# Kernel tuning notes

Hardware: AMD Instinct MI355X
Metric: run time of the kernel (lower is better)

The kernel has to match this reference:

```python
import jax, jax.numpy as jnp
import numpy as np

MAX_RADIUS = 0.9
TEMP = 0.1

def _to_poincare(x, W, b):
    # Linear + Tanh, then rescale into Poincare ball of radius 0.9
    h = jnp.tanh(x @ W.T + b)
    norm = jnp.clip(jnp.linalg.norm(h, axis=-1, keepdims=True), 1e-8, None)
    scale = jnp.where(norm > MAX_RADIUS, MAX_RADIUS / norm, jnp.ones_like(norm))
    return h * scale

def setup_inputs() -> dict:
    key = jax.random.key(0)
    kq, kw, kb, km, ko = jax.random.split(key, 5)
    B, N, D = 2048, 100000, 128
    return {
        "query": jax.random.normal(kq, (B, D), dtype=jnp.float32),
        "W": jax.random.normal(kw, (D, D), dtype=jnp.float32) * (1.0 / np.sqrt(D)),
        "b": jax.random.normal(kb, (D,), dtype=jnp.float32) * 0.01,
        "mem_emb": jax.random.normal(km, (N, D), dtype=jnp.float32),
        "mem_out": jax.random.normal(ko, (N, D), dtype=jnp.float32),
        "k": 16,
    }

def reference(query, W, b, mem_emb, mem_out, k):
    q = _to_poincare(query, W, b)          # [B, D]
    m = _to_poincare(mem_emb, W, b)        # [N, D]
    # Euclidean cdist via the GEMM form: ||q||^2 + ||m||^2 - 2 q.m
    q2 = jnp.sum(q * q, axis=-1, keepdims=True)           # [B, 1]
    m2 = jnp.sum(m * m, axis=-1)                          # [N]
    d2 = q2 + m2[None, :] - 2.0 * (q @ m.T)               # [B, N]
    dists = jnp.sqrt(jnp.maximum(d2, 1e-12))
    # k smallest distances
    neg_top, top_idx = jax.lax.top_k(-dists, k)           # [B, k]
    top_dists = -neg_top
    weights = jax.nn.softmax(-top_dists / TEMP, axis=-1)  # [B, k]
    outcomes = mem_out[top_idx]                           # [B, k, D]
    return weights, outcomes
```

## Files before the change

### kernel.cpp

```cpp
#include <hip/hip_runtime.h>
#include <hip/hip_bf16.h>
#include <math.h>

#define DIM 128
#define QB 64
#define MB 64
#define NSPLIT 32
#define KSEL 16
#define KOWN 4
#define RESCORE 32
#define IDXMASK 0x1FFFu
#define KEYMASK 0xFFFFE000u

using bf16x8 = __attribute__((ext_vector_type(8))) short;
using f32x4  = __attribute__((ext_vector_type(4))) float;

__device__ inline unsigned short f2bf(float f) {
  __hip_bfloat16 h = __float2bfloat16(f);
  return __builtin_bit_cast(unsigned short, h);
}
__device__ inline unsigned uminu(unsigned a, unsigned b) {
  return __builtin_elementwise_min(a, b);
}
__device__ inline unsigned umaxu(unsigned a, unsigned b) {
  return __builtin_elementwise_max(a, b);
}
__device__ inline unsigned long long umin64(unsigned long long a,
                                            unsigned long long b) {
  return __builtin_elementwise_min(a, b);
}

__device__ inline f32x4 mfma16(bf16x8 a, bf16x8 b, f32x4 c) {
  return __builtin_amdgcn_mfma_f32_16x16x32_bf16(a, b, c, 0, 0, 0);
}

__device__ inline void gload_lds16(const void* g, void* l) {
  __builtin_amdgcn_global_load_lds(
      (const __attribute__((address_space(1))) void*)g,
      (__attribute__((address_space(3))) void*)l, 16, 0, 0);
}

__global__ __launch_bounds__(512) void poincare2_k(
    const float* __restrict__ Xm, int Rm,
    const float* __restrict__ Xq, int Rq,
    const float* __restrict__ W, const float* __restrict__ bias,
    float* __restrict__ Pm, float* __restrict__ Pm2,
    float* __restrict__ Pm2s, int npadm,
    unsigned short* __restrict__ Pmbf,
    float* __restrict__ Pq, float* __restrict__ Pq2, int nbm)
{
  __shared__ float Wl[DIM * DIM];
  __shared__ float nrm[128 * 17];
  __shared__ float norm2l[128];

  const int t  = threadIdx.x;
  const int cg = t & 15;
  const int rg = t >> 4;

  const bool ismem = (int)blockIdx.x < nbm;
  const float* X = ismem ? Xm : Xq;
  const int    R = ismem ? Rm : Rq;
  float*       P  = ismem ? Pm  : Pq;
  float*       P2 = ismem ? Pm2 : Pq2;
  unsigned short* Pbf = ismem ? Pmbf : nullptr;
  const int rbase = (ismem ? blockIdx.x : (blockIdx.x - nbm)) * 128;

  for (int i = t; i < DIM * 32; i += 512) {
    const int j = i >> 5, c = i & 31;
    const float4 v = *(const float4*)&W[j * DIM + c * 4];
    *(float4*)&Wl[j * DIM + ((c ^ ((j >> 3) & 7)) << 2)] = v;
  }
  float bj[8];
  #pragma unroll
  for (int u = 0; u < 8; ++u) bj[u] = bias[cg * 8 + u];

  const float* xr[4];
  #pragma unroll
  for (int v = 0; v < 4; ++v) {
    int row = rbase + rg + 32 * v;
    if (row > R - 1) row = R - 1;
    xr[v] = X + (size_t)row * DIM;
  }
  __syncthreads();

  float acc[4][8];
  #pragma unroll
  for (int v = 0; v < 4; ++v)
    #pragma unroll
    for (int u = 0; u < 8; ++u) acc[v][u] = bj[u];

  #pragma unroll 2
  for (int k4 = 0; k4 < 32; ++k4) {
    float4 xv[4], wv[8];
    #pragma unroll
    for (int v = 0; v < 4; ++v) xv[v] = *(const float4*)&xr[v][k4 * 4];
    #pragma unroll
    for (int u = 0; u < 8; ++u) {
      const int j = cg * 8 + u;
      wv[u] = *(const float4*)&Wl[j * DIM + ((k4 ^ ((j >> 3) & 7)) << 2)];
    }
    #pragma unroll
    for (int v = 0; v < 4; ++v)
      #pragma unroll
      for (int u = 0; u < 8; ++u) {
        acc[v][u] = fmaf(xv[v].x, wv[u].x, acc[v][u]);
        acc[v][u] = fmaf(xv[v].y, wv[u].y, acc[v][u]);
        acc[v][u] = fmaf(xv[v].z, wv[u].z, acc[v][u]);
        acc[v][u] = fmaf(xv[v].w, wv[u].w, acc[v][u]);
      }
  }

  #pragma unroll
  for (int v = 0; v < 4; ++v) {
    float pn = 0.f;
    #pragma unroll
    for (int u = 0; u < 8; ++u) {
      const float th = tanhf(acc[v][u]);
      acc[v][u] = th;
      pn = fmaf(th, th, pn);
    }
    nrm[(rg + 32 * v) * 17 + cg] = pn;
  }
  __syncthreads();
  if (t < 128) {
    float s = 0.f;
    #pragma unroll
    for (int c2 = 0; c2 < 16; ++c2) s += nrm[t * 17 + c2];
    norm2l[t] = s;
    const int row = rbase + t;
    if (row < R) {
      const float nm = sqrtf(s);
      const float sc = (nm > 0.9f) ? (0.9f / nm) : 1.0f;
      const float p2v = s * sc * sc;
      P2[row] = p2v;
      if (ismem) Pm2s[row] = fmaf(0.5f, p2v, 1.0f);
    } else if (ismem && row < npadm) {
      Pm2s[row] = __int_as_float(0x7f800000);
    }
  }
  __syncthreads();

  #pragma unroll
  for (int v = 0; v < 4; ++v) {
    const int r = rg + 32 * v;
    const int row = rbase + r;
    if (row < R) {
      const float n2 = norm2l[r];
      const float nm = sqrtf(n2);
      const float sc = (nm > 0.9f) ? (0.9f / nm) : 1.0f;
      float o[8];
      #pragma unroll
      for (int u = 0; u < 8; ++u) o[u] = acc[v][u] * sc;
      *(float4*)&P[(size_t)row * DIM + cg * 8]     = make_float4(o[0], o[1], o[2], o[3]);
      *(float4*)&P[(size_t)row * DIM + cg * 8 + 4] = make_float4(o[4], o[5], o[6], o[7]);
      if (Pbf) {
        uint4 pb;
        pb.x = (unsigned)f2bf(o[0]) | ((unsigned)f2bf(o[1]) << 16);
        pb.y = (unsigned)f2bf(o[2]) | ((unsigned)f2bf(o[3]) << 16);
        pb.z = (unsigned)f2bf(o[4]) | ((unsigned)f2bf(o[5]) << 16);
        pb.w = (unsigned)f2bf(o[6]) | ((unsigned)f2bf(o[7]) << 16);
        *(uint4*)&Pmbf[(size_t)row * DIM + ((cg ^ (row & 15)) << 3)] = pb;
      }
    }
  }
}

template<bool USEBF>
__global__ __launch_bounds__(512, 8) void score_topk_k(
    const float* __restrict__ Pq,
    const float* __restrict__ Pm, const float* __restrict__ Pm2s,
    const unsigned short* __restrict__ Pmbf,
    int N, int splitlen, unsigned* __restrict__ splitTop)
{
  __shared__ __align__(16) unsigned short Ml0[MB * DIM];
  __shared__ __align__(16) unsigned short Ml1[MB * DIM];

  const int t = threadIdx.x;
  const int lane = t & 63;
  const int w = t >> 6, wr = w >> 1, wc = w & 1;
  const int split = blockIdx.x;
  const int qbase = blockIdx.y * QB;
  const int mlo = split * splitlen;
  const int mhi = min(mlo + splitlen, N);

  bf16x8 qf[4];
  {
    const int qrow = qbase + wr * 16 + (lane & 15);
    #pragma unroll
    for (int ks = 0; ks < 4; ++ks) {
      const float* src = &Pq[(size_t)qrow * DIM + ks * 32 + (lane >> 4) * 8];
      float4 lo = *(const float4*)src;
      float4 hi = *(const float4*)(src + 4);
      bf16x8 v;
      v[0] = (short)f2bf(-lo.x); v[1] = (short)f2bf(-lo.y);
      v[2] = (short)f2bf(-lo.z); v[3] = (short)f2bf(-lo.w);
      v[4] = (short)f2bf(-hi.x); v[5] = (short)f2bf(-hi.y);
      v[6] = (short)f2bf(-hi.z); v[7] = (short)f2bf(-hi.w);
      qf[ks] = v;
    }
  }

  const size_t soff0 = (size_t)(w * 8 + (lane >> 4)) * DIM + ((lane & 15) << 3);
  const size_t soff1 = soff0 + 4 * DIM;
  unsigned short* const d00 = &Ml0[(w * 8) * DIM];
  unsigned short* const d01 = &Ml0[(w * 8 + 4) * DIM];
  unsigned short* const d10 = &Ml1[(w * 8) * DIM];
  unsigned short* const d11 = &Ml1[(w * 8 + 4) * DIM];

  auto stage = [&](int mbase, unsigned short* dA, unsigned short* dB,
                   unsigned short* lds) {
    if constexpr (USEBF) {
      const unsigned short* b = Pmbf + (size_t)mbase * DIM;
      gload_lds16(b + soff0, dA);
      gload_lds16(b + soff1, dB);
    } else {
      const int fr = t >> 3, fe = t & 7;
      const float* src = Pm + (size_t)(mbase + fr) * DIM + fe * 16;
      float4 a0 = *(const float4*)(src + 0);
      float4 a1 = *(const float4*)(src + 4);
      float4 a2 = *(const float4*)(src + 8);
      float4 a3 = *(const float4*)(src + 12);
      uint4 o0, o1;
      o0.x = (unsigned)f2bf(a0.x) | ((unsigned)f2bf(a0.y) << 16);
      o0.y = (unsigned)f2bf(a0.z) | ((unsigned)f2bf(a0.w) << 16);
      o0.z = (unsigned)f2bf(a1.x) | ((unsigned)f2bf(a1.y) << 16);
      o0.w = (unsigned)f2bf(a1.z) | ((unsigned)f2bf(a1.w) << 16);
      o1.x = (unsigned)f2bf(a2.x) | ((unsigned)f2bf(a2.y) << 16);
      o1.y = (unsigned)f2bf(a2.z) | ((unsigned)f2bf(a2.w) << 16);
      o1.z = (unsigned)f2bf(a3.x) | ((unsigned)f2bf(a3.y) << 16);
      o1.w = (unsigned)f2bf(a3.z) | ((unsigned)f2bf(a3.w) << 16);
      char* base = (char*)lds + fr * 256;
      *(uint4*)(base + (((2 * fe)     ^ (fr & 15)) << 4)) = o0;
      *(uint4*)(base + (((2 * fe + 1) ^ (fr & 15)) << 4)) = o1;
    }
  };

  const int ntiles = (mhi - mlo + MB - 1) / MB;
  const int mcol = wc * 32 + (lane & 15);

  stage(mlo, d00, d01, Ml0);
  float ca = Pm2s[mlo + mcol];
  float cb = Pm2s[mlo + mcol + 16];
  float caN, cbN;
  __syncthreads();

  unsigned keys[4][KOWN];
  #pragma unroll
  for (int r = 0; r < 4; ++r)
    #pragma unroll
    for (int i = 0; i < KOWN; ++i) keys[r][i] = 0xFFFFFFFFu;

  auto body = [&](int tile, const unsigned short* ldsCur,
                  unsigned short* dA, unsigned short* dB, unsigned short* ldsNxt,
                  float ca_, float cb_, float& caN_, float& cbN_) {
    const int mbase = mlo + tile * MB;
    const bool more = (tile + 1 < ntiles);
    if (more) {
      stage(mbase + MB, dA, dB, ldsNxt);
      caN_ = Pm2s[mbase + MB + mcol];
      cbN_ = Pm2s[mbase + MB + mcol + 16];
    }

    f32x4 acc0 = (f32x4){ca_, ca_, ca_, ca_};
    f32x4 acc1 = (f32x4){cb_, cb_, cb_, cb_};

    const int rowA = mcol;
    const int rowB = mcol + 16;
    __builtin_amdgcn_s_setprio(1);
    #pragma unroll
    for (int ks = 0; ks < 4; ++ks) {
      const int kb = ks * 64 + (lane >> 4) * 16;
      bf16x8 bfrA = *(const bf16x8*)((const char*)ldsCur + rowA * 256 +
                                     (kb ^ ((rowA & 15) << 4)));
      bf16x8 bfrB = *(const bf16x8*)((const char*)ldsCur + rowB * 256 +
                                     (kb ^ ((rowB & 15) << 4)));
      acc0 = mfma16(qf[ks], bfrA, acc0);
      acc1 = mfma16(qf[ks], bfrB, acc1);
    }
    __builtin_amdgcn_s_setprio(0);

    const unsigned idx0 = (unsigned)(tile * MB + mcol);
    #pragma unroll
    for (int r = 0; r < 4; ++r) {
      {
        unsigned c = (__float_as_uint(acc0[r]) & KEYMASK) | idx0;
        #pragma unroll
        for (int i = 0; i < KOWN; ++i) {
          const unsigned lo = uminu(c, keys[r][i]);
          c = umaxu(c, keys[r][i]);
          keys[r][i] = lo;
        }
      }
      {
        unsigned c = (__float_as_uint(acc1[r]) & KEYMASK) | (idx0 + 16);
        #pragma unroll
        for (int i = 0; i < KOWN; ++i) {
          const unsigned lo = uminu(c, keys[r][i]);
          c = umaxu(c, keys[r][i]);
          keys[r][i] = lo;
        }
      }
    }
    __syncthreads();
  };

  int tile = 0;
  while (true) {
    body(tile, Ml0, d10, d11, Ml1, ca, cb, caN, cbN); if (++tile == ntiles) break;
    body(tile, Ml1, d00, d01, Ml0, caN, cbN, ca, cb); if (++tile == ntiles) break;
  }

  #pragma unroll
  for (int r = 0; r < 4; ++r) {
    unsigned k0 = keys[r][0], k1 = keys[r][1];
    unsigned k2 = keys[r][2], k3 = keys[r][3];
    unsigned out = 0xFFFFFFFFu;
    for (int round = 0; round < 8; ++round) {
      unsigned g = k0;
      g = uminu(g, __shfl_xor(g, 1, 16));
      g = uminu(g, __shfl_xor(g, 2, 16));
      g = uminu(g, __shfl_xor(g, 4, 16));
      g = uminu(g, __shfl_xor(g, 8, 16));
      const bool mine = (k0 == g);
      k0 = mine ? k1 : k0;
      k1 = mine ? k2 : k1;
      k2 = mine ? k3 : k2;
      k3 = mine ? 0xFFFFFFFFu : k3;
      if ((lane & 15) == round) out = g;
    }
    const int q = qbase + wr * 16 + (lane >> 4) * 4 + r;
    if ((lane & 15) < 8)
      splitTop[(((size_t)q * NSPLIT + split) * 2 + wc) * 8 + (lane & 15)] = out;
  }
}

__global__ __launch_bounds__(256) void finalize_k(
    const unsigned* __restrict__ splitTop,
    const float* __restrict__ Pq, const float* __restrict__ Pq2,
    const float* __restrict__ Pm, const float* __restrict__ Pm2,
    const float* __restrict__ memOut, int N, int splitlen,
    float* __restrict__ outW, float* __restrict__ outO)
{
  const int wv   = threadIdx.x >> 6;
  const int lane = threadIdx.x & 63;
  const int q = blockIdx.x * 4 + wv;

  __shared__ unsigned      sKey[4][RESCORE];
  __shared__ unsigned char sSrc[4][RESCORE];
  __shared__ unsigned long long sKeyx[4][RESCORE];
  __shared__ unsigned long long sSel[4][KSEL];
  __shared__ float sEl[4][KSEL];

  {
    const unsigned* gp = splitTop + (size_t)q * (NSPLIT * 2 * 8) + lane * 8;
    unsigned a[8];
    uint4 lo = *(const uint4*)gp;
    uint4 hi = *(const uint4*)(gp + 4);
    a[0] = lo.x; a[1] = lo.y; a[2] = lo.z; a[3] = lo.w;
    a[4] = hi.x; a[5] = hi.y; a[6] = hi.z; a[7] = hi.w;
    for (int r = 0; r < RESCORE; ++r) {
      unsigned g = a[0];
      g = uminu(g, __shfl_xor(g, 1));
      g = uminu(g, __shfl_xor(g, 2));
      g = uminu(g, __shfl_xor(g, 4));
      g = uminu(g, __shfl_xor(g, 8));
      g = uminu(g, __shfl_xor(g, 16));
      g = uminu(g, __shfl_xor(g, 32));
      unsigned long long mask = __ballot(a[0] == g);
      const int fl = __ffsll((unsigned long long)mask) - 1;
      if (lane == fl) {
        #pragma unroll
        for (int i = 0; i < 7; ++i) a[i] = a[i + 1];
        a[7] = 0xFFFFFFFFu;
      }
      if (lane == 0) { sKey[wv][r] = g; sSrc[wv][r] = (unsigned char)fl; }
    }
  }

  #pragma unroll
  for (int p = 0; p < 4; ++p) {
    const int g8 = p * 8 + (lane >> 3), e = lane & 7;
    const int src = sSrc[wv][g8];
    const int gidx = (src >> 1) * splitlen + (int)(sKey[wv][g8] & IDXMASK);
    const float4* qr = (const float4*)&Pq[(size_t)q * DIM];
    const float4* mr = (const float4*)&Pm[(size_t)gidx * DIM];
    float s = 0.f;
    #pragma unroll
    for (int u = 0; u < 4; ++u) {
      float4 a = qr[e * 4 + u], b = mr[e * 4 + u];
      s = fmaf(a.x, b.x, s); s = fmaf(a.y, b.y, s);
      s = fmaf(a.z, b.z, s); s = fmaf(a.w, b.w, s);
    }
    s += __shfl_xor(s, 1, 8);
    s += __shfl_xor(s, 2, 8);
    s += __shfl_xor(s, 4, 8);
    if (e == 0) {
      float d2 = (Pq2[q] + Pm2[gidx]) - 2.0f * s;
      float dist = sqrtf(fmaxf(d2, 1e-12f));
      sKeyx[wv][g8] =
          (((unsigned long long)__float_as_uint(dist)) << 32) | (unsigned)gidx;
    }
  }

  {
    unsigned long long kk = (lane < RESCORE) ? sKeyx[wv][lane] : ~0ull;
    for (int r = 0; r < KSEL; ++r) {
      unsigned long long g = kk;
      g = umin64(g, __shfl_xor(g, 1));
      g = umin64(g, __shfl_xor(g, 2));
      g = umin64(g, __shfl_xor(g, 4));
      g = umin64(g, __shfl_xor(g, 8));
      g = umin64(g, __shfl_xor(g, 16));
      g = umin64(g, __shfl_xor(g, 32));
      if (kk == g) kk = ~0ull;
      if (lane == 0) sSel[wv][r] = g;
    }
  }

  if (lane < KSEL) {
    const float d  = __uint_as_float((unsigned)(sSel[wv][lane] >> 32));
    const float d0 = __uint_as_float((unsigned)(sSel[wv][0] >> 32));
    sEl[wv][lane] = expf((d0 - d) * 10.0f);
  }
  if (lane < KSEL) {
    float sum = 0.f;
    #pragma unroll
    for (int i = 0; i < KSEL; ++i) sum += sEl[wv][i];
    outW[(size_t)q * KSEL + lane] = sEl[wv][lane] / sum;
  }

  #pragma unroll
  for (int i = 0; i < 8; ++i) {
    const int f4 = lane + i * 64;
    const int r = f4 >> 5, c4 = f4 & 31;
    const int idx = (int)(sSel[wv][r] & 0xffffffffu);
    *(float4*)&outO[((size_t)q * KSEL + r) * DIM + c4 * 4] =
        *(const float4*)&memOut[(size_t)idx * DIM + c4 * 4];
  }
}

extern "C" void kernel_launch(void* const* d_in, const int* in_sizes, int n_in,
                              void* d_out, int out_size, void* d_ws, size_t ws_size,
                              hipStream_t stream)
{
  const float* query   = (const float*)d_in[0];
  const float* W       = (const float*)d_in[1];
  const float* bias    = (const float*)d_in[2];
  const float* mem_emb = (const float*)d_in[3];
  const float* mem_out = (const float*)d_in[4];
  const int B = in_sizes[0] / DIM;
  const int N = in_sizes[3] / DIM;
  const int N_pad = ((N + MB + 15) / 16) * 16;

  const int splitlen = ((N + NSPLIT * MB - 1) / (NSPLIT * MB)) * MB;

  float* ws  = (float*)d_ws;
  float* Pm  = ws;
  float* Pm2 = Pm + (size_t)N_pad * DIM;
  float* Pm2s = Pm2 + N_pad;
  float* Pq  = Pm2s + N_pad;
  float* Pq2 = Pq + (size_t)B * DIM;
  unsigned* splitTop = (unsigned*)(Pq2 + B);
  unsigned short* Pmbf = (unsigned short*)(splitTop + (size_t)B * NSPLIT * 2 * 8);
  const size_t need_bf = (size_t)((char*)(Pmbf + (size_t)N_pad * DIM) - (char*)d_ws);
  const bool usebf = ws_size >= need_bf;

  float* outW = (float*)d_out;
  float* outO = outW + (size_t)B * KSEL;

  const int nbm = (N + 127) / 128;
  const int nbq = (B + 127) / 128;
  poincare2_k<<<dim3(nbm + nbq), dim3(512), 0, stream>>>(
      mem_emb, N, query, B, W, bias, Pm, Pm2, Pm2s, N_pad,
      usebf ? Pmbf : nullptr, Pq, Pq2, nbm);

  dim3 grid2(NSPLIT, B / QB);
  if (usebf)
    score_topk_k<true><<<grid2, dim3(512), 0, stream>>>(Pq, Pm, Pm2s, Pmbf, N,
                                                        splitlen, splitTop);
  else
    score_topk_k<false><<<grid2, dim3(512), 0, stream>>>(Pq, Pm, Pm2s, nullptr, N,
                                                         splitlen, splitTop);

  finalize_k<<<dim3(B / 4), dim3(256), 0, stream>>>(splitTop, Pq, Pq2, Pm, Pm2,
                                                    mem_out, N, splitlen,
                                                    outW, outO);
}
```

Baseline: 231.6 us.

## Double query tile per block, triple-buffer memory tiles, preload norms into LDS

```diff
diff --git a/kernel.cpp b/kernel.cpp
--- a/kernel.cpp
+++ b/kernel.cpp
@@ -3,7 +3,7 @@
 #include <math.h>
 
 #define DIM 128
-#define QB 64
+#define QB 128
 #define MB 64
 #define NSPLIT 32
 #define KSEL 16
@@ -11,6 +11,7 @@
 #define RESCORE 32
 #define IDXMASK 0x1FFFu
 #define KEYMASK 0xFFFFE000u
+#define M2MAX 3200
 
 using bf16x8 = __attribute__((ext_vector_type(8))) short;
 using f32x4  = __attribute__((ext_vector_type(4))) float;
@@ -38,6 +39,15 @@
   __builtin_amdgcn_global_load_lds(
       (const __attribute__((address_space(1))) void*)g,
       (__attribute__((address_space(3))) void*)l, 16, 0, 0);
+}
+
+__device__ inline void ins4(unsigned (&ks)[KOWN], unsigned c) {
+  #pragma unroll
+  for (int i = 0; i < KOWN; ++i) {
+    const unsigned lo = uminu(c, ks[i]);
+    c = umaxu(c, ks[i]);
+    ks[i] = lo;
+  }
 }
 
 __global__ __launch_bounds__(512) void poincare2_k(
@@ -166,14 +176,14 @@
 }
 
 template<bool USEBF>
-__global__ __launch_bounds__(512, 8) void score_topk_k(
+__global__ __launch_bounds__(512, 4) void score_topk_k(
     const float* __restrict__ Pq,
     const float* __restrict__ Pm, const float* __restrict__ Pm2s,
     const unsigned short* __restrict__ Pmbf,
     int N, int splitlen, unsigned* __restrict__ splitTop)
 {
-  __shared__ __align__(16) unsigned short Ml0[MB * DIM];
-  __shared__ __align__(16) unsigned short Ml1[MB * DIM];
+  __shared__ __align__(16) unsigned short Ml[3][MB * DIM];
+  __shared__ float m2all[M2MAX];
 
   const int t = threadIdx.x;
   const int lane = t & 63;
@@ -182,10 +192,12 @@
   const int qbase = blockIdx.y * QB;
   const int mlo = split * splitlen;
   const int mhi = min(mlo + splitlen, N);
-
-  bf16x8 qf[4];
-  {
-    const int qrow = qbase + wr * 16 + (lane & 15);
+  const int ntiles = (mhi - mlo + MB - 1) / MB;
+
+  bf16x8 qf[2][4];
+  #pragma unroll
+  for (int s = 0; s < 2; ++s) {
+    const int qrow = qbase + wr * 32 + s * 16 + (lane & 15);
     #pragma unroll
     for (int ks = 0; ks < 4; ++ks) {
       const float* src = &Pq[(size_t)qrow * DIM + ks * 32 + (lane >> 4) * 8];
@@ -196,142 +208,140 @@
       v[2] = (short)f2bf(-lo.z); v[3] = (short)f2bf(-lo.w);
       v[4] = (short)f2bf(-hi.x); v[5] = (short)f2bf(-hi.y);
       v[6] = (short)f2bf(-hi.z); v[7] = (short)f2bf(-hi.w);
-      qf[ks] = v;
-    }
-  }
+      qf[s][ks] = v;
+    }
+  }
+
+  for (int i = t; i < splitlen; i += 512) m2all[i] = Pm2s[mlo + i];
 
   const size_t soff0 = (size_t)(w * 8 + (lane >> 4)) * DIM + ((lane & 15) << 3);
   const size_t soff1 = soff0 + 4 * DIM;
-  unsigned short* const d00 = &Ml0[(w * 8) * DIM];
-  unsigned short* const d01 = &Ml0[(w * 8 + 4) * DIM];
-  unsigned short* const d10 = &Ml1[(w * 8) * DIM];
-  unsigned short* const d11 = &Ml1[(w * 8 + 4) * DIM];
-
-  auto stage = [&](int mbase, unsigned short* dA, unsigned short* dB,
-                   unsigned short* lds) {
-    if constexpr (USEBF) {
-      const unsigned short* b = Pmbf + (size_t)mbase * DIM;
-      gload_lds16(b + soff0, dA);
-      gload_lds16(b + soff1, dB);
-    } else {
-      const int fr = t >> 3, fe = t & 7;
-      const float* src = Pm + (size_t)(mbase + fr) * DIM + fe * 16;
-      float4 a0 = *(const float4*)(src + 0);
-      float4 a1 = *(const float4*)(src + 4);
-      float4 a2 = *(const float4*)(src + 8);
-      float4 a3 = *(const float4*)(src + 12);
-      uint4 o0, o1;
-      o0.x = (unsigned)f2bf(a0.x) | ((unsigned)f2bf(a0.y) << 16);
-      o0.y = (unsigned)f2bf(a0.z) | ((unsigned)f2bf(a0.w) << 16);
-      o0.z = (unsigned)f2bf(a1.x) | ((unsigned)f2bf(a1.y) << 16);
-      o0.w = (unsigned)f2bf(a1.z) | ((unsigned)f2bf(a1.w) << 16);
-      o1.x = (unsigned)f2bf(a2.x) | ((unsigned)f2bf(a2.y) << 16);
-      o1.y = (unsigned)f2bf(a2.z) | ((unsigned)f2bf(a2.w) << 16);
-      o1.z = (unsigned)f2bf(a3.x) | ((unsigned)f2bf(a3.y) << 16);
-      o1.w = (unsigned)f2bf(a3.z) | ((unsigned)f2bf(a3.w) << 16);
-      char* base = (char*)lds + fr * 256;
-      *(uint4*)(base + (((2 * fe)     ^ (fr & 15)) << 4)) = o0;
-      *(uint4*)(base + (((2 * fe + 1) ^ (fr & 15)) << 4)) = o1;
-    }
+
+  auto stageU = [&](int tilei, int buf) {
+    const unsigned short* b = Pmbf + (size_t)(mlo + tilei * MB) * DIM;
+    gload_lds16(b + soff0, &Ml[buf][(w * 8) * DIM]);
+    gload_lds16(b + soff1, &Ml[buf][(w * 8 + 4) * DIM]);
   };
-
-  const int ntiles = (mhi - mlo + MB - 1) / MB;
+  uint4 sv0, sv1;
+  auto stageF_load = [&](int tilei) {
+    const int fr = t >> 3, fe = t & 7;
+    const float* src = Pm + (size_t)(mlo + tilei * MB + fr) * DIM + fe * 16;
+    float4 a0 = *(const float4*)(src + 0);
+    float4 a1 = *(const float4*)(src + 4);
+    float4 a2 = *(const float4*)(src + 8);
+    float4 a3 = *(const float4*)(src + 12);
+    sv0.x = (unsigned)f2bf(a0.x) | ((unsigned)f2bf(a0.y) << 16);
+    sv0.y = (unsigned)f2bf(a0.z) | ((unsigned)f2bf(a0.w) << 16);
+    sv0.z = (unsigned)f2bf(a1.x) | ((unsigned)f2bf(a1.y) << 16);
+    sv0.w = (unsigned)f2bf(a1.z) | ((unsigned)f2bf(a1.w) << 16);
+    sv1.x = (unsigned)f2bf(a2.x) | ((unsigned)f2bf(a2.y) << 16);
+    sv1.y = (unsigned)f2bf(a2.z) | ((unsigned)f2bf(a2.w) << 16);
+    sv1.z = (unsigned)f2bf(a3.x) | ((unsigned)f2bf(a3.y) << 16);
+    sv1.w = (unsigned)f2bf(a3.z) | ((unsigned)f2bf(a3.w) << 16);
+  };
+  auto stageF_write = [&](int buf) {
+    const int fr = t >> 3, fe = t & 7;
+    char* base = (char*)&Ml[buf][0] + fr * 256;
+    *(uint4*)(base + (((2 * fe)     ^ (fr & 15)) << 4)) = sv0;
+    *(uint4*)(base + (((2 * fe + 1) ^ (fr & 15)) << 4)) = sv1;
+  };
+
+  unsigned keys[2][4][KOWN];
+  #pragma unroll
+  for (int s = 0; s < 2; ++s)
+    #pragma unroll
+    for (int r = 0; r < 4; ++r)
+      #pragma unroll
+      for (int i = 0; i < KOWN; ++i) keys[s][r][i] = 0xFFFFFFFFu;
+
   const int mcol = wc * 32 + (lane & 15);
-
-  stage(mlo, d00, d01, Ml0);
-  float ca = Pm2s[mlo + mcol];
-  float cb = Pm2s[mlo + mcol + 16];
-  float caN, cbN;
-  __syncthreads();
-
-  unsigned keys[4][KOWN];
-  #pragma unroll
-  for (int r = 0; r < 4; ++r)
-    #pragma unroll
-    for (int i = 0; i < KOWN; ++i) keys[r][i] = 0xFFFFFFFFu;
-
-  auto body = [&](int tile, const unsigned short* ldsCur,
-                  unsigned short* dA, unsigned short* dB, unsigned short* ldsNxt,
-                  float ca_, float cb_, float& caN_, float& cbN_) {
-    const int mbase = mlo + tile * MB;
-    const bool more = (tile + 1 < ntiles);
-    if (more) {
-      stage(mbase + MB, dA, dB, ldsNxt);
-      caN_ = Pm2s[mbase + MB + mcol];
-      cbN_ = Pm2s[mbase + MB + mcol + 16];
-    }
-
-    f32x4 acc0 = (f32x4){ca_, ca_, ca_, ca_};
-    f32x4 acc1 = (f32x4){cb_, cb_, cb_, cb_};
-
-    const int rowA = mcol;
-    const int rowB = mcol + 16;
+  const int rowA = mcol, rowB = mcol + 16;
+
+  auto compute = [&](int tile, const unsigned short* cur) {
+    const float ca = m2all[tile * MB + mcol];
+    const float cb = m2all[tile * MB + mcol + 16];
+    f32x4 a00 = (f32x4){ca, ca, ca, ca};
+    f32x4 a01 = (f32x4){cb, cb, cb, cb};
+    f32x4 a10 = (f32x4){ca, ca, ca, ca};
+    f32x4 a11 = (f32x4){cb, cb, cb, cb};
     __builtin_amdgcn_s_setprio(1);
     #pragma unroll
     for (int ks = 0; ks < 4; ++ks) {
       const int kb = ks * 64 + (lane >> 4) * 16;
-      bf16x8 bfrA = *(const bf16x8*)((const char*)ldsCur + rowA * 256 +
+      bf16x8 bfrA = *(const bf16x8*)((const char*)cur + rowA * 256 +
                                      (kb ^ ((rowA & 15) << 4)));
-      bf16x8 bfrB = *(const bf16x8*)((const char*)ldsCur + rowB * 256 +
+      bf16x8 bfrB = *(const bf16x8*)((const char*)cur + rowB * 256 +
                                      (kb ^ ((rowB & 15) << 4)));
-      acc0 = mfma16(qf[ks], bfrA, acc0);
-      acc1 = mfma16(qf[ks], bfrB, acc1);
+      a00 = mfma16(qf[0][ks], bfrA, a00);
+      a01 = mfma16(qf[0][ks], bfrB, a01);
+      a10 = mfma16(qf[1][ks], bfrA, a10);
+      a11 = mfma16(qf[1][ks], bfrB, a11);
     }
     __builtin_amdgcn_s_setprio(0);
-
     const unsigned idx0 = (unsigned)(tile * MB + mcol);
     #pragma unroll
     for (int r = 0; r < 4; ++r) {
-      {
-        unsigned c = (__float_as_uint(acc0[r]) & KEYMASK) | idx0;
-        #pragma unroll
-        for (int i = 0; i < KOWN; ++i) {
-          const unsigned lo = uminu(c, keys[r][i]);
-          c = umaxu(c, keys[r][i]);
-          keys[r][i] = lo;
-        }
+      ins4(keys[0][r], (__float_as_uint(a00[r]) & KEYMASK) | idx0);
+      ins4(keys[0][r], (__float_as_uint(a01[r]) & KEYMASK) | (idx0 + 16));
+      ins4(keys[1][r], (__float_as_uint(a10[r]) & KEYMASK) | idx0);
+      ins4(keys[1][r], (__float_as_uint(a11[r]) & KEYMASK) | (idx0 + 16));
+    }
+  };
+
+  if constexpr (USEBF) {
+    __syncthreads();
+    stageU(0, 0);
+    if (ntiles > 1) stageU(1, 1);
+    int cur = 0;
+    for (int i = 0; i < ntiles; ++i) {
+      if (i < ntiles - 1) asm volatile("s_waitcnt vmcnt(2)" ::: "memory");
+      else                asm volatile("s_waitcnt vmcnt(0)" ::: "memory");
+      __builtin_amdgcn_s_barrier();
+      __builtin_amdgcn_sched_barrier(0);
+      int nb = cur + 2; if (nb >= 3) nb -= 3;
+      if (i + 2 < ntiles) stageU(i + 2, nb);
+      compute(i, &Ml[cur][0]);
+      cur = (cur + 1 == 3) ? 0 : cur + 1;
+    }
+  } else {
+    stageF_load(0);
+    stageF_write(0);
+    __syncthreads();
+    for (int i = 0; i < ntiles; ++i) {
+      const int cur = i & 1;
+      const bool more = (i + 1 < ntiles);
+      if (more) stageF_load(i + 1);
+      compute(i, &Ml[cur][0]);
+      __syncthreads();
+      if (more) stageF_write(cur ^ 1);
+      __syncthreads();
+    }
+  }
+
+  #pragma unroll
+  for (int s = 0; s < 2; ++s)
+    #pragma unroll
+    for (int r = 0; r < 4; ++r) {
+      unsigned k0 = keys[s][r][0], k1 = keys[s][r][1];
+      unsigned k2 = keys[s][r][2], k3 = keys[s][r][3];
+      unsigned out = 0xFFFFFFFFu;
+      for (int round = 0; round < 8; ++round) {
+        unsigned g = k0;
+        g = uminu(g, __shfl_xor(g, 1, 16));
+        g = uminu(g, __shfl_xor(g, 2, 16));
+        g = uminu(g, __shfl_xor(g, 4, 16));
+        g = uminu(g, __shfl_xor(g, 8, 16));
+        const bool mine = (k0 == g);
+        k0 = mine ? k1 : k0;
+        k1 = mine ? k2 : k1;
+        k2 = mine ? k3 : k2;
+        k3 = mine ? 0xFFFFFFFFu : k3;
+        if ((lane & 15) == round) out = g;
       }
-      {
-        unsigned c = (__float_as_uint(acc1[r]) & KEYMASK) | (idx0 + 16);
-        #pragma unroll
-        for (int i = 0; i < KOWN; ++i) {
-          const unsigned lo = uminu(c, keys[r][i]);
-          c = umaxu(c, keys[r][i]);
-          keys[r][i] = lo;
-        }
-      }
-    }
-    __syncthreads();
-  };
-
-  int tile = 0;
-  while (true) {
-    body(tile, Ml0, d10, d11, Ml1, ca, cb, caN, cbN); if (++tile == ntiles) break;
-    body(tile, Ml1, d00, d01, Ml0, caN, cbN, ca, cb); if (++tile == ntiles) break;
-  }
-
-  #pragma unroll
-  for (int r = 0; r < 4; ++r) {
-    unsigned k0 = keys[r][0], k1 = keys[r][1];
-    unsigned k2 = keys[r][2], k3 = keys[r][3];
-    unsigned out = 0xFFFFFFFFu;
-    for (int round = 0; round < 8; ++round) {
-      unsigned g = k0;
-      g = uminu(g, __shfl_xor(g, 1, 16));
-      g = uminu(g, __shfl_xor(g, 2, 16));
-      g = uminu(g, __shfl_xor(g, 4, 16));
-      g = uminu(g, __shfl_xor(g, 8, 16));
-      const bool mine = (k0 == g);
-      k0 = mine ? k1 : k0;
-      k1 = mine ? k2 : k1;
-      k2 = mine ? k3 : k2;
-      k3 = mine ? 0xFFFFFFFFu : k3;
-      if ((lane & 15) == round) out = g;
-    }
-    const int q = qbase + wr * 16 + (lane >> 4) * 4 + r;
-    if ((lane & 15) < 8)
-      splitTop[(((size_t)q * NSPLIT + split) * 2 + wc) * 8 + (lane & 15)] = out;
-  }
+      const int q = qbase + wr * 32 + s * 16 + (lane >> 4) * 4 + r;
+      if ((lane & 15) < 8)
+        splitTop[(((size_t)q * NSPLIT + split) * 2 + wc) * 8 + (lane & 15)] = out;
+    }
 }
 
 __global__ __launch_bounds__(256) void finalize_k(
@@ -450,28 +460,28 @@
   const float* mem_out = (const float*)d_in[4];
   const int B = in_sizes[0] / DIM;
   const int N = in_sizes[3] / DIM;
-  const int N_pad = ((N + MB + 15) / 16) * 16;
 
   const int splitlen = ((N + NSPLIT * MB - 1) / (NSPLIT * MB)) * MB;
+  const int N_pad2 = NSPLIT * splitlen;
 
   float* ws  = (float*)d_ws;
   float* Pm  = ws;
-  float* Pm2 = Pm + (size_t)N_pad * DIM;
-  float* Pm2s = Pm2 + N_pad;
-  float* Pq  = Pm2s + N_pad;
+  float* Pm2 = Pm + (size_t)N_pad2 * DIM;
+  float* Pm2s = Pm2 + N_pad2;
+  float* Pq  = Pm2s + N_pad2;
   float* Pq2 = Pq + (size_t)B * DIM;
   unsigned* splitTop = (unsigned*)(Pq2 + B);
   unsigned short* Pmbf = (unsigned short*)(splitTop + (size_t)B * NSPLIT * 2 * 8);
-  const size_t need_bf = (size_t)((char*)(Pmbf + (size_t)N_pad * DIM) - (char*)d_ws);
+  const size_t need_bf = (size_t)((char*)(Pmbf + (size_t)N_pad2 * DIM) - (char*)d_ws);
   const bool usebf = ws_size >= need_bf;
 
   float* outW = (float*)d_out;
   float* outO = outW + (size_t)B * KSEL;
 
-  const int nbm = (N + 127) / 128;
+  const int nbm = (N_pad2 + 127) / 128;
   const int nbq = (B + 127) / 128;
   poincare2_k<<<dim3(nbm + nbq), dim3(512), 0, stream>>>(
-      mem_emb, N, query, B, W, bias, Pm, Pm2, Pm2s, N_pad,
+      mem_emb, N, query, B, W, bias, Pm, Pm2, Pm2s, N_pad2,
       usebf ? Pmbf : nullptr, Pq, Pq2, nbm);
 
   dim3 grid2(NSPLIT, B / QB);
```

Measured after the change: 211.6 us. 1.09x faster.
